# Kernel tuning notes

Hardware: AMD Instinct MI355X
Metric: run time of the kernel (lower is better)

## Reference

```python
import jax, jax.numpy as jnp
import numpy as np

B, T, D, H, A = 1024, 128, 64, 256, 8  # batch, seq_len, state_dim, hidden_dim, action_dim


def setup_inputs() -> dict:
    key = jax.random.key(0)
    ks = jax.random.split(key, 12)
    k = 1.0 / np.sqrt(H)  # PyTorch LSTM/Linear default init range
    u = lambda kk, shape: jax.random.uniform(kk, shape, jnp.float32, -k, k)
    return {
        "state": jax.random.normal(ks[0], (B, 1, D), jnp.float32),
        "gamma": jnp.ones((D,), jnp.float32),
        "beta": jnp.zeros((D,), jnp.float32),
        "W_ih0": u(ks[1], (4 * H, D)),
        "W_hh0": u(ks[2], (4 * H, H)),
        "b_ih0": u(ks[3], (4 * H,)),
        "b_hh0": u(ks[4], (4 * H,)),
        "W_ih1": u(ks[5], (4 * H, H)),
        "W_hh1": u(ks[6], (4 * H, H)),
        "b_ih1": u(ks[7], (4 * H,)),
        "b_hh1": u(ks[8], (4 * H,)),
        "fcW": u(ks[9], (A, H)),
        "fcb": u(ks[10], (A,)),
        "seq_len": T,
    }


def _lstm_cell(x, h, c, Wih, Whh, b):
    # PyTorch gate order: input, forget, cell(g), output
    g = x @ Wih.T + h @ Whh.T + b
    i, f, gg, o = jnp.split(g, 4, axis=-1)
    c_new = jax.nn.sigmoid(f) * c + jax.nn.sigmoid(i) * jnp.tanh(gg)
    h_new = jax.nn.sigmoid(o) * jnp.tanh(c_new)
    return h_new, c_new


def reference(state, gamma, beta, W_ih0, W_hh0, b_ih0, b_hh0,
              W_ih1, W_hh1, b_ih1, b_hh1, fcW, fcb, seq_len):
    # state: [B, 1, D]; the same (layernormed) input is fed every timestep,
    # only the LSTM hidden/cell state evolves.
    x = state[:, 0, :]  # [B, D]
    mu = x.mean(-1, keepdims=True)
    var = ((x - mu) ** 2).mean(-1, keepdims=True)
    xn = (x - mu) * jax.lax.rsqrt(var + 1e-5) * gamma + beta  # LayerNorm(state_dim)

    b0 = b_ih0 + b_hh0
    b1 = b_ih1 + b_hh1
    bsz = x.shape[0]
    hdim = W_hh0.shape[1]
    z = jnp.zeros((bsz, hdim), x.dtype)
    init = (z, z, z, z)  # (h0, c0, h1, c1); h=None -> zeros in torch

    def step(carry, _):
        h0, c0, h1, c1 = carry
        h0, c0 = _lstm_cell(xn, h0, c0, W_ih0, W_hh0, b0)  # layer 0
        h1, c1 = _lstm_cell(h0, h1, c1, W_ih1, W_hh1, b1)  # layer 1
        action = jnp.tanh(h1 @ fcW.T + fcb)  # [B, A]
        return (h0, c0, h1, c1), action

    _, actions = jax.lax.scan(step, init, None, length=seq_len)  # [T, B, A]
    return jnp.transpose(actions, (1, 0, 2))  # [B, T, A]
```

## Files before the change

kernel.cpp:

```cpp
#include <hip/hip_runtime.h>
#include <math.h>

#define B_    1024
#define T_    128
#define D_    64
#define H_    256
#define A_    8

#define NG    8
#define NB    32
#define MB    128
#define SL    8
#define FSTR  32

typedef __attribute__((ext_vector_type(8))) short short8;
typedef __attribute__((ext_vector_type(4))) float floatx4;

__device__ __forceinline__ short f2bf(float f) {
    union { float f; unsigned u; } x; x.f = f;
    return (short)((x.u + 0x7FFFu + ((x.u >> 16) & 1u)) >> 16);
}
__device__ __forceinline__ float bf2f(short s) {
    union { unsigned u; float f; } x;
    x.u = ((unsigned)(unsigned short)s) << 16;
    return x.f;
}
__device__ __forceinline__ float sigm(float x) {
    return __builtin_amdgcn_rcpf(1.0f + __expf(-x));
}
__device__ __forceinline__ float ftanh(float x) {
    float t = __expf(-2.0f * fabsf(x));
    float r = (1.0f - t) * __builtin_amdgcn_rcpf(1.0f + t);
    return copysignf(r, x);
}

__device__ __forceinline__ void cell_update(floatx4 aA, floatx4 aB, float* cpair,
                                            short* __restrict__ Hw, size_t rowbase,
                                            int colbase, int hi, int rsel) {
    floatx4 tA, tB;
#pragma unroll
    for (int r = 0; r < 4; ++r) {
        tA[r] = __shfl_xor(aA[r], 8, 64);
        tB[r] = __shfl_xor(aB[r], 8, 64);
    }
#pragma unroll
    for (int rr = 0; rr < 2; ++rr) {
        int r = rsel + rr;
        float gi = hi ? tA[r] : aA[r];
        float gf = hi ? aA[r] : tA[r];
        float gg = hi ? tB[r] : aB[r];
        float go = hi ? aB[r] : tB[r];
        float cn = sigm(gf) * cpair[rr] + sigm(gi) * ftanh(gg);
        float hn = sigm(go) * ftanh(cn);
        cpair[rr] = cn;
        Hw[(rowbase + r) * H_ + colbase] = f2bf(hn);
    }
}

__global__ void __launch_bounds__(256)
actor_kernel(const float* __restrict__ state, const float* __restrict__ gamma,
             const float* __restrict__ beta,  const float* __restrict__ Wih0,
             const float* __restrict__ Whh0,  const float* __restrict__ bih0,
             const float* __restrict__ bhh0,  const float* __restrict__ Wih1,
             const float* __restrict__ Whh1,  const float* __restrict__ bih1,
             const float* __restrict__ bhh1,  const float* __restrict__ fcW,
             const float* __restrict__ fcb,   float* __restrict__ out,
             unsigned* __restrict__ flags, unsigned* __restrict__ aux,
             short* __restrict__ Hb0, short* __restrict__ Hb1)
{
    __shared__ __attribute__((aligned(16))) short sWp[28672];
    __shared__ int sMap[3];

    const int blk  = blockIdx.x;
    const int tid  = threadIdx.x;
    const int lane = tid & 63;
    const int wave = tid >> 6;

    if (tid == 0) {
        unsigned xcc;
        asm volatile("s_getreg_b32 %0, hwreg(HW_REG_XCC_ID)" : "=s"(xcc));
        xcc &= 7u;
        unsigned r = atomicAdd(&aux[xcc * 16], 1u);
        __hip_atomic_fetch_add(&aux[256], 1u, __ATOMIC_ACQ_REL,
                               __HIP_MEMORY_SCOPE_AGENT);
        while (__hip_atomic_load(&aux[256], __ATOMIC_RELAXED,
                                 __HIP_MEMORY_SCOPE_AGENT) < (unsigned)gridDim.x)
            __builtin_amdgcn_s_sleep(1);
        __builtin_amdgcn_fence(__ATOMIC_ACQUIRE, "agent");
        int pre = 0, tot = 0; bool ok = true;
        for (int x = 0; x < 8; ++x) {
            int cx = (int)__hip_atomic_load(&aux[x * 16], __ATOMIC_RELAXED,
                                            __HIP_MEMORY_SCOPE_AGENT);
            if (cx & 31) ok = false;
            if (x < (int)xcc) pre += cx >> 5;
            tot += cx >> 5;
        }
        if (tot != NG) ok = false;
        sMap[0] = ok ? (pre + (int)(r >> 5)) : (blk & 7);
        sMap[1] = ok ? (int)(r & 31)         : (blk >> 3);
        sMap[2] = ok ? 1 : 0;
    }
    __syncthreads();
    const int  g     = sMap[0];
    const int  s     = sMap[1];
    const bool fastp = (sMap[2] != 0);
    const int  g128  = g * MB;

    const int q4   = lane >> 4;
    const int l15  = lane & 15;
    const int jj   = l15 & 7;
    const int hi   = l15 >> 3;
    const int rg0  = hi * H_ + s * SL + jj;
    const int rg1  = (2 + hi) * H_ + s * SL + jj;
    const int mrow = wave * 16 + q4 * 4;
    const int colbase = s * SL + jj;
    const int rsel = hi * 2;

    float* sXn = (float*)sWp;
    if (tid < MB) {
        const float* xr = state + (size_t)(g128 + tid) * D_;
        float mu = 0.f;
        for (int d = 0; d < D_; ++d) mu += xr[d];
        mu *= (1.0f / D_);
        float var = 0.f;
        for (int d = 0; d < D_; ++d) { float t = xr[d] - mu; var += t * t; }
        var *= (1.0f / D_);
        float is = rsqrtf(var + 1e-5f);
        for (int d = 0; d < D_; ++d)
            sXn[tid * 65 + d] = (xr[d] - mu) * is * gamma[d] + beta[d];
    }
    __syncthreads();

    const float b0v0 = bih0[rg0] + bhh0[rg0];
    const float b0v1 = bih0[rg1] + bhh0[rg1];
    const float b1v0 = bih1[rg0] + bhh1[rg0];
    const float b1v1 = bih1[rg1] + bhh1[rg1];

    floatx4 pre0a[2], pre0b[2];
    {
        const float* w0 = Wih0 + (size_t)rg0 * D_;
        const float* w1 = Wih0 + (size_t)rg1 * D_;
#pragma unroll
        for (int u = 0; u < 2; ++u)
#pragma unroll
            for (int r = 0; r < 4; ++r) { pre0a[u][r] = b0v0; pre0b[u][r] = b0v1; }
        for (int d = 0; d < D_; ++d) {
            float wa = w0[d], wb = w1[d];
#pragma unroll
            for (int u = 0; u < 2; ++u)
#pragma unroll
                for (int r = 0; r < 4; ++r) {
                    float xv = sXn[(u * 64 + mrow + r) * 65 + d];
                    pre0a[u][r] += xv * wa;
                    pre0b[u][r] += xv * wb;
                }
        }
    }
    __syncthreads();

    const int fo = lane >> 3, fk8 = lane & 7;
    float fcw_r[32];
#pragma unroll
    for (int kk = 0; kk < 32; ++kk) fcw_r[kk] = fcW[fo * H_ + fk8 * 32 + kk];
    const float fcb_r = fcb[fo];

    for (int idx = tid; idx < 8192; idx += 256) {
        int kt = idx >> 10, rem = idx & 1023;
        int c = rem >> 9, rem2 = rem & 511;
        int ln = rem2 >> 3, j = rem2 & 7;
        int q4_ = ln >> 4, l15_ = ln & 15;
        int n = c * 16 + l15_;
        int r = (n >> 3) * H_ + s * SL + (n & 7);
        int k = kt * 32 + q4_ * 8 + j;
        sWp[idx] = f2bf(Whh0[(size_t)r * H_ + k]);
    }
    for (int idx = tid; idx < 16384; idx += 256) {
        int kt = idx >> 11, rem = idx & 2047;
        int c = rem >> 9, rem2 = rem & 511;
        int ln = rem2 >> 3, j = rem2 & 7;
        int q4_ = ln >> 4, l15_ = ln & 15;
        int n = (c & 1) * 16 + l15_;
        int r = (n >> 3) * H_ + s * SL + (n & 7);
        int k = kt * 32 + q4_ * 8 + j;
        float v = (c >> 1) ? Whh1[(size_t)r * H_ + k] : Wih1[(size_t)r * H_ + k];
        sWp[8192 + idx] = f2bf(v);
    }
    float c0[2][2] = {{0.f,0.f},{0.f,0.f}}, c1[2][2] = {{0.f,0.f},{0.f,0.f}};
    __syncthreads();

    const short* ldsB0 = sWp + lane * 8;
    const short* ldsB1 = sWp + 8192 + lane * 8;

    const int BH = B_ * H_;
    for (int ph = 0; ph <= T_ + 1; ++ph) {
        const short* H0r  = Hb0 + ((ph + 1) & 1) * BH;
        short*       H0w  = Hb0 + (ph & 1) * BH;
        const short* H1r2 = Hb1 + (ph & 1) * BH;
        short*       H1w  = Hb1 + ((ph + 1) & 1) * BH;

        const bool doL0 = (ph < T_);
        const bool doL1 = (ph >= 1 && ph <= T_);

        if (ph >= 2) {
            int t = ph - 2;
            int b = 4 * s + wave;
            const short8* hp = (const short8*)(H1r2 + (size_t)(g128 + b) * H_ + fk8 * 32);
            float sum = 0.f;
#pragma unroll
            for (int c8 = 0; c8 < 4; ++c8) {
                short8 hv = hp[c8];
#pragma unroll
                for (int j = 0; j < 8; ++j)
                    sum += bf2f(hv[j]) * fcw_r[c8 * 8 + j];
            }
            sum += __shfl_down(sum, 4, 8);
            sum += __shfl_down(sum, 2, 8);
            sum += __shfl_down(sum, 1, 8);
            if (fk8 == 0)
                out[((size_t)(g128 + b) * T_ + t) * A_ + fo] = ftanh(sum + fcb_r);
        }

        if (doL0 || doL1) {
#pragma unroll
            for (int u = 0; u < 2; ++u) {
                short8 a0[8], a1[8];
                const size_t arow = (size_t)(g128 + u * 64 + wave * 16 + l15) * H_ + q4 * 8;
                const short* ap = H0r + arow;
#pragma unroll
                for (int kt = 0; kt < 8; ++kt)
                    a0[kt] = *(const short8*)(ap + kt * 32);
                if (doL1) {
                    const short* cp = H1r2 + arow;
#pragma unroll
                    for (int kt = 0; kt < 8; ++kt)
                        a1[kt] = *(const short8*)(cp + kt * 32);
                }

                floatx4 l0a = pre0a[u], l0b = pre0b[u], l1a, l1b;
#pragma unroll
                for (int r = 0; r < 4; ++r) { l1a[r] = b1v0; l1b[r] = b1v1; }

#pragma unroll
                for (int kt = 0; kt < 8; ++kt) {
                    if (doL0) {
                        short8 b0a = *(const short8*)(ldsB0 + kt * 1024);
                        short8 b0b = *(const short8*)(ldsB0 + kt * 1024 + 512);
                        l0a = __builtin_amdgcn_mfma_f32_16x16x32_bf16(a0[kt], b0a, l0a, 0, 0, 0);
                        l0b = __builtin_amdgcn_mfma_f32_16x16x32_bf16(a0[kt], b0b, l0b, 0, 0, 0);
                    }
                    if (doL1) {
                        short8 bia = *(const short8*)(ldsB1 + kt * 2048);
                        short8 bib = *(const short8*)(ldsB1 + kt * 2048 + 512);
                        short8 bha = *(const short8*)(ldsB1 + kt * 2048 + 1024);
                        short8 bhb = *(const short8*)(ldsB1 + kt * 2048 + 1536);
                        l1a = __builtin_amdgcn_mfma_f32_16x16x32_bf16(a0[kt], bia, l1a, 0, 0, 0);
                        l1b = __builtin_amdgcn_mfma_f32_16x16x32_bf16(a0[kt], bib, l1b, 0, 0, 0);
                        l1a = __builtin_amdgcn_mfma_f32_16x16x32_bf16(a1[kt], bha, l1a, 0, 0, 0);
                        l1b = __builtin_amdgcn_mfma_f32_16x16x32_bf16(a1[kt], bhb, l1b, 0, 0, 0);
                    }
                }

                size_t rowbase = (size_t)(g128 + u * 64 + mrow);
                if (doL0) cell_update(l0a, l0b, c0[u], H0w, rowbase, colbase, hi, rsel);
                if (doL1) cell_update(l1a, l1b, c1[u], H1w, rowbase, colbase, hi, rsel);
            }
        }

        if (ph <= T_) {
            __syncthreads();
            const unsigned val = (unsigned)(ph + 2);
            if (tid == 0) {
                if (!fastp) __builtin_amdgcn_fence(__ATOMIC_RELEASE, "agent");
                __hip_atomic_store(&flags[(g * NB + s) * FSTR], val,
                                   __ATOMIC_RELAXED, __HIP_MEMORY_SCOPE_AGENT);
            }
            if (wave == 0 && lane < NB) {
                while (__hip_atomic_load(&flags[(g * NB + lane) * FSTR],
                                         __ATOMIC_RELAXED, __HIP_MEMORY_SCOPE_AGENT)
                       < val)
                    __builtin_amdgcn_s_sleep(1);
            }
            __syncthreads();
            if (fastp) { asm volatile("buffer_inv sc0" ::: "memory"); }
            else       { __builtin_amdgcn_fence(__ATOMIC_ACQUIRE, "agent"); }
        }
    }
}

extern "C" void kernel_launch(void* const* d_in, const int* in_sizes, int n_in,
                              void* d_out, int out_size, void* d_ws, size_t ws_size,
                              hipStream_t stream)
{
    const float* state = (const float*)d_in[0];
    const float* gamma = (const float*)d_in[1];
    const float* beta  = (const float*)d_in[2];
    const float* Wih0  = (const float*)d_in[3];
    const float* Whh0  = (const float*)d_in[4];
    const float* bih0  = (const float*)d_in[5];
    const float* bhh0  = (const float*)d_in[6];
    const float* Wih1  = (const float*)d_in[7];
    const float* Whh1  = (const float*)d_in[8];
    const float* bih1  = (const float*)d_in[9];
    const float* bhh1  = (const float*)d_in[10];
    const float* fcW   = (const float*)d_in[11];
    const float* fcb   = (const float*)d_in[12];
    float* out = (float*)d_out;

    unsigned* flags = (unsigned*)d_ws;
    unsigned* aux   = (unsigned*)((char*)d_ws + 32768);
    short* Hb0 = (short*)((char*)d_ws + 36864);
    short* Hb1 = Hb0 + 2 * B_ * H_;

    size_t zbytes = 36864 + (size_t)4 * B_ * H_ * sizeof(short);
    hipMemsetAsync(d_ws, 0, zbytes, stream);

    void* args[] = { &state, &gamma, &beta, &Wih0, &Whh0, &bih0, &bhh0,
                     &Wih1, &Whh1, &bih1, &bhh1, &fcW, &fcb, &out,
                     &flags, &aux, &Hb0, &Hb1 };
    hipError_t err = hipLaunchCooperativeKernel((const void*)actor_kernel,
                                                dim3(NG * NB), dim3(256),
                                                args, 0, stream);
    if (err != hipSuccess) {
        (void)hipGetLastError();
        actor_kernel<<<dim3(NG * NB), dim3(256), 0, stream>>>(
            state, gamma, beta, Wih0, Whh0, bih0, bhh0,
            Wih1, Whh1, bih1, bhh1, fcW, fcb, out, flags, aux, Hb0, Hb1);
    }
    (void)in_sizes; (void)n_in; (void)out_size; (void)ws_size;
}
```

Baseline: 1.095 ms.

## Split batch into 64-row groups across 512 blocks with register-held layer-0 weights

Templates the kernel on rows per block, so that with two blocks per CU it launches 512 blocks, each handling 64 batch rows instead of 128. To shrink LDS to 32KB and allow two resident blocks, the layer-0 recurrent weights move from LDS into per-lane registers, and only the layer-1 weights stay in LDS. The flag stride is halved and the flag polling moves to wave 3. This halves the serial per-step work per block, at the cost of more blocks taking part in each group barrier and higher register pressure, which could cut occupancy.

```diff
diff --git a/kernel.cpp b/kernel.cpp
--- a/kernel.cpp
+++ b/kernel.cpp
@@ -7,11 +7,9 @@
 #define H_    256
 #define A_    8
 
-#define NG    8
 #define NB    32
-#define MB    128
 #define SL    8
-#define FSTR  32
+#define FSTR  16
 
 typedef __attribute__((ext_vector_type(8))) short short8;
 typedef __attribute__((ext_vector_type(4))) float floatx4;
@@ -57,6 +55,7 @@
     }
 }
 
+template<int UH>
 __global__ void __launch_bounds__(256)
 actor_kernel(const float* __restrict__ state, const float* __restrict__ gamma,
              const float* __restrict__ beta,  const float* __restrict__ Wih0,
@@ -68,14 +67,18 @@
              unsigned* __restrict__ flags, unsigned* __restrict__ aux,
              short* __restrict__ Hb0, short* __restrict__ Hb1)
 {
-    __shared__ __attribute__((aligned(16))) short sWp[28672];
-    __shared__ int sMap[3];
+    constexpr int NGROUPS = 16 / UH;
+    constexpr int M       = 64 * UH;
+    constexpr int FCR     = 2 * UH;
+
+    __shared__ __attribute__((aligned(16))) short sWp[16384];
 
     const int blk  = blockIdx.x;
     const int tid  = threadIdx.x;
     const int lane = tid & 63;
     const int wave = tid >> 6;
 
+    int* sMapi = (int*)sWp;
     if (tid == 0) {
         unsigned xcc;
         asm volatile("s_getreg_b32 %0, hwreg(HW_REG_XCC_ID)" : "=s"(xcc));
@@ -95,16 +98,17 @@
             if (x < (int)xcc) pre += cx >> 5;
             tot += cx >> 5;
         }
-        if (tot != NG) ok = false;
-        sMap[0] = ok ? (pre + (int)(r >> 5)) : (blk & 7);
-        sMap[1] = ok ? (int)(r & 31)         : (blk >> 3);
-        sMap[2] = ok ? 1 : 0;
+        if (tot != NGROUPS) ok = false;
+        sMapi[0] = ok ? (pre + (int)(r >> 5)) : (blk % NGROUPS);
+        sMapi[1] = ok ? (int)(r & 31)         : (blk / NGROUPS);
+        sMapi[2] = ok ? 1 : 0;
     }
     __syncthreads();
-    const int  g     = sMap[0];
-    const int  s     = sMap[1];
-    const bool fastp = (sMap[2] != 0);
-    const int  g128  = g * MB;
+    const int  g     = sMapi[0];
+    const int  s     = sMapi[1];
+    const bool fastp = (sMapi[2] != 0);
+    __syncthreads();
+    const int gM = g * M;
 
     const int q4   = lane >> 4;
     const int l15  = lane & 15;
@@ -116,47 +120,44 @@
     const int colbase = s * SL + jj;
     const int rsel = hi * 2;
 
-    float* sXn = (float*)sWp;
-    if (tid < MB) {
-        const float* xr = state + (size_t)(g128 + tid) * D_;
-        float mu = 0.f;
-        for (int d = 0; d < D_; ++d) mu += xr[d];
-        mu *= (1.0f / D_);
-        float var = 0.f;
-        for (int d = 0; d < D_; ++d) { float t = xr[d] - mu; var += t * t; }
-        var *= (1.0f / D_);
-        float is = rsqrtf(var + 1e-5f);
-        for (int d = 0; d < D_; ++d)
-            sXn[tid * 65 + d] = (xr[d] - mu) * is * gamma[d] + beta[d];
-    }
-    __syncthreads();
-
     const float b0v0 = bih0[rg0] + bhh0[rg0];
     const float b0v1 = bih0[rg1] + bhh0[rg1];
     const float b1v0 = bih1[rg0] + bhh1[rg0];
     const float b1v1 = bih1[rg1] + bhh1[rg1];
 
-    floatx4 pre0a[2], pre0b[2];
+    floatx4 pre0a[UH], pre0b[UH];
+    float* sXn = (float*)sWp;
     {
         const float* w0 = Wih0 + (size_t)rg0 * D_;
         const float* w1 = Wih0 + (size_t)rg1 * D_;
-#pragma unroll
-        for (int u = 0; u < 2; ++u)
+        for (int u = 0; u < UH; ++u) {
+            if (tid < 64) {
+                const float* xr = state + (size_t)(gM + u * 64 + tid) * D_;
+                float mu = 0.f;
+                for (int d = 0; d < D_; ++d) mu += xr[d];
+                mu *= (1.0f / D_);
+                float var = 0.f;
+                for (int d = 0; d < D_; ++d) { float t = xr[d] - mu; var += t * t; }
+                var *= (1.0f / D_);
+                float is = rsqrtf(var + 1e-5f);
+                for (int d = 0; d < D_; ++d)
+                    sXn[tid * 65 + d] = (xr[d] - mu) * is * gamma[d] + beta[d];
+            }
+            __syncthreads();
 #pragma unroll
             for (int r = 0; r < 4; ++r) { pre0a[u][r] = b0v0; pre0b[u][r] = b0v1; }
-        for (int d = 0; d < D_; ++d) {
-            float wa = w0[d], wb = w1[d];
-#pragma unroll
-            for (int u = 0; u < 2; ++u)
+            for (int d = 0; d < D_; ++d) {
+                float wa = w0[d], wb = w1[d];
 #pragma unroll
                 for (int r = 0; r < 4; ++r) {
-                    float xv = sXn[(u * 64 + mrow + r) * 65 + d];
+                    float xv = sXn[(mrow + r) * 65 + d];
                     pre0a[u][r] += xv * wa;
                     pre0b[u][r] += xv * wb;
                 }
-        }
-    }
-    __syncthreads();
+            }
+            __syncthreads();
+        }
+    }
 
     const int fo = lane >> 3, fk8 = lane & 7;
     float fcw_r[32];
@@ -164,16 +165,23 @@
     for (int kk = 0; kk < 32; ++kk) fcw_r[kk] = fcW[fo * H_ + fk8 * 32 + kk];
     const float fcb_r = fcb[fo];
 
-    for (int idx = tid; idx < 8192; idx += 256) {
-        int kt = idx >> 10, rem = idx & 1023;
-        int c = rem >> 9, rem2 = rem & 511;
-        int ln = rem2 >> 3, j = rem2 & 7;
-        int q4_ = ln >> 4, l15_ = ln & 15;
-        int n = c * 16 + l15_;
-        int r = (n >> 3) * H_ + s * SL + (n & 7);
-        int k = kt * 32 + q4_ * 8 + j;
-        sWp[idx] = f2bf(Whh0[(size_t)r * H_ + k]);
-    }
+    short8 bw0[16];
+    {
+        const float* wA = Whh0 + (size_t)rg0 * H_ + q4 * 8;
+        const float* wB = Whh0 + (size_t)rg1 * H_ + q4 * 8;
+#pragma unroll
+        for (int kt = 0; kt < 8; ++kt) {
+            short8 sa, sb;
+#pragma unroll
+            for (int j = 0; j < 8; ++j) {
+                sa[j] = f2bf(wA[kt * 32 + j]);
+                sb[j] = f2bf(wB[kt * 32 + j]);
+            }
+            bw0[2 * kt]     = sa;
+            bw0[2 * kt + 1] = sb;
+        }
+    }
+
     for (int idx = tid; idx < 16384; idx += 256) {
         int kt = idx >> 11, rem = idx & 2047;
         int c = rem >> 9, rem2 = rem & 511;
@@ -183,13 +191,13 @@
         int r = (n >> 3) * H_ + s * SL + (n & 7);
         int k = kt * 32 + q4_ * 8 + j;
         float v = (c >> 1) ? Whh1[(size_t)r * H_ + k] : Wih1[(size_t)r * H_ + k];
-        sWp[8192 + idx] = f2bf(v);
-    }
-    float c0[2][2] = {{0.f,0.f},{0.f,0.f}}, c1[2][2] = {{0.f,0.f},{0.f,0.f}};
+        sWp[idx] = f2bf(v);
+    }
+    float c0[UH][2], c1[UH][2];
+    for (int u = 0; u < UH; ++u) { c0[u][0]=c0[u][1]=0.f; c1[u][0]=c1[u][1]=0.f; }
     __syncthreads();
 
-    const short* ldsB0 = sWp + lane * 8;
-    const short* ldsB1 = sWp + 8192 + lane * 8;
+    const short* ldsB1 = sWp + lane * 8;
 
     const int BH = B_ * H_;
     for (int ph = 0; ph <= T_ + 1; ++ph) {
@@ -201,10 +209,10 @@
         const bool doL0 = (ph < T_);
         const bool doL1 = (ph >= 1 && ph <= T_);
 
-        if (ph >= 2) {
+        if (ph >= 2 && wave < FCR) {
             int t = ph - 2;
-            int b = 4 * s + wave;
-            const short8* hp = (const short8*)(H1r2 + (size_t)(g128 + b) * H_ + fk8 * 32);
+            int b = FCR * s + wave;
+            const short8* hp = (const short8*)(H1r2 + (size_t)(gM + b) * H_ + fk8 * 32);
             float sum = 0.f;
 #pragma unroll
             for (int c8 = 0; c8 < 4; ++c8) {
@@ -217,14 +225,13 @@
             sum += __shfl_down(sum, 2, 8);
             sum += __shfl_down(sum, 1, 8);
             if (fk8 == 0)
-                out[((size_t)(g128 + b) * T_ + t) * A_ + fo] = ftanh(sum + fcb_r);
+                out[((size_t)(gM + b) * T_ + t) * A_ + fo] = ftanh(sum + fcb_r);
         }
 
         if (doL0 || doL1) {
-#pragma unroll
-            for (int u = 0; u < 2; ++u) {
+            for (int u = 0; u < UH; ++u) {
                 short8 a0[8], a1[8];
-                const size_t arow = (size_t)(g128 + u * 64 + wave * 16 + l15) * H_ + q4 * 8;
+                const size_t arow = (size_t)(gM + u * 64 + wave * 16 + l15) * H_ + q4 * 8;
                 const short* ap = H0r + arow;
 #pragma unroll
                 for (int kt = 0; kt < 8; ++kt)
@@ -243,10 +250,8 @@
 #pragma unroll
                 for (int kt = 0; kt < 8; ++kt) {
                     if (doL0) {
-                        short8 b0a = *(const short8*)(ldsB0 + kt * 1024);
-                        short8 b0b = *(const short8*)(ldsB0 + kt * 1024 + 512);
-                        l0a = __builtin_amdgcn_mfma_f32_16x16x32_bf16(a0[kt], b0a, l0a, 0, 0, 0);
-                        l0b = __builtin_amdgcn_mfma_f32_16x16x32_bf16(a0[kt], b0b, l0b, 0, 0, 0);
+                        l0a = __builtin_amdgcn_mfma_f32_16x16x32_bf16(a0[kt], bw0[2*kt],   l0a, 0, 0, 0);
+                        l0b = __builtin_amdgcn_mfma_f32_16x16x32_bf16(a0[kt], bw0[2*kt+1], l0b, 0, 0, 0);
                     }
                     if (doL1) {
                         short8 bia = *(const short8*)(ldsB1 + kt * 2048);
@@ -260,7 +265,7 @@
                     }
                 }
 
-                size_t rowbase = (size_t)(g128 + u * 64 + mrow);
+                size_t rowbase = (size_t)(gM + u * 64 + mrow);
                 if (doL0) cell_update(l0a, l0b, c0[u], H0w, rowbase, colbase, hi, rsel);
                 if (doL1) cell_update(l1a, l1b, c1[u], H1w, rowbase, colbase, hi, rsel);
             }
@@ -274,7 +279,7 @@
                 __hip_atomic_store(&flags[(g * NB + s) * FSTR], val,
                                    __ATOMIC_RELAXED, __HIP_MEMORY_SCOPE_AGENT);
             }
-            if (wave == 0 && lane < NB) {
+            if (wave == 3 && lane < NB) {
                 while (__hip_atomic_load(&flags[(g * NB + lane) * FSTR],
                                          __ATOMIC_RELAXED, __HIP_MEMORY_SCOPE_AGENT)
                        < val)
@@ -317,14 +322,32 @@
     void* args[] = { &state, &gamma, &beta, &Wih0, &Whh0, &bih0, &bhh0,
                      &Wih1, &Whh1, &bih1, &bhh1, &fcW, &fcb, &out,
                      &flags, &aux, &Hb0, &Hb1 };
-    hipError_t err = hipLaunchCooperativeKernel((const void*)actor_kernel,
-                                                dim3(NG * NB), dim3(256),
-                                                args, 0, stream);
-    if (err != hipSuccess) {
-        (void)hipGetLastError();
-        actor_kernel<<<dim3(NG * NB), dim3(256), 0, stream>>>(
-            state, gamma, beta, Wih0, Whh0, bih0, bhh0,
-            Wih1, Whh1, bih1, bhh1, fcW, fcb, out, flags, aux, Hb0, Hb1);
+
+    int nb = 0;
+    hipError_t qe = hipOccupancyMaxActiveBlocksPerMultiprocessor(
+        &nb, (const void*)(actor_kernel<1>), 256, 0);
+    if (qe != hipSuccess) { (void)hipGetLastError(); nb = 0; }
+
+    if (nb >= 2) {
+        hipError_t err = hipLaunchCooperativeKernel((const void*)(actor_kernel<1>),
+                                                    dim3(512), dim3(256),
+                                                    args, 0, stream);
+        if (err != hipSuccess) {
+            (void)hipGetLastError();
+            actor_kernel<1><<<dim3(512), dim3(256), 0, stream>>>(
+                state, gamma, beta, Wih0, Whh0, bih0, bhh0,
+                Wih1, Whh1, bih1, bhh1, fcW, fcb, out, flags, aux, Hb0, Hb1);
+        }
+    } else {
+        hipError_t err = hipLaunchCooperativeKernel((const void*)(actor_kernel<2>),
+                                                    dim3(256), dim3(256),
+                                                    args, 0, stream);
+        if (err != hipSuccess) {
+            (void)hipGetLastError();
+            actor_kernel<2><<<dim3(256), dim3(256), 0, stream>>>(
+                state, gamma, beta, Wih0, Whh0, bih0, bhh0,
+                Wih1, Whh1, bih1, bhh1, fcW, fcb, out, flags, aux, Hb0, Hb1);
+        }
     }
     (void)in_sizes; (void)n_in; (void)out_size; (void)ws_size;
 }
```

Measured after the change: 1.133 ms. 3.5% more time.
